# Kernel optimization log

Measured on AMD Instinct MI355X. Metric: run time of the kernel, lower is better.

Reference implementation:

```python
import jax, jax.numpy as jnp
import numpy as np

N_CUMULANTS = 3  # forward() calls compute_cumulants_fwd(values, 3)
P = 576
N_ROWS = 200000
PROJ_DIMS = 4


def setup_inputs() -> dict:
    key = jax.random.key(0)
    k1, k2, k3 = jax.random.split(key, 3)
    X = jax.random.normal(k1, (N_ROWS, P), dtype=jnp.float32)
    mu = jax.random.normal(k2, (P * N_CUMULANTS,), dtype=jnp.float32)
    W = jax.random.normal(k3, (P * N_CUMULANTS, PROJ_DIMS), dtype=jnp.float32)
    return {"X": X, "mu": mu, "W": W}


def _cumulants(X):
    # X: (N, P). Vectorized version of the per-column torch loop.
    # n_cumulants = 3: c0 = mean, c1 = mean(centered^1), c2 = mean(centered^2)
    m = jnp.mean(X, axis=0)                 # (P,)
    centered = X - m                        # (N, P)
    mom1 = jnp.mean(centered, axis=0)       # (P,) ~0 numerically, kept for faithfulness
    mom2 = jnp.mean(centered * centered, axis=0)  # (P,) variance
    # layout matches out[:, jbase:jbase+n_cumulants]: interleave per feature column
    c = jnp.stack([m, mom1, mom2], axis=1)  # (P, 3)
    return c.reshape(1, -1)                 # (1, P*3)


def reference(X, mu, W):
    cum = _cumulants(X.astype(jnp.float32))          # (1, P*3)
    projected = jnp.einsum('ij,jk->ik', cum - mu, W)  # (1, PROJ_DIMS)
    return projected
```

## Files before the change

kernel.cpp:

```cpp
#include <hip/hip_runtime.h>

#define N_ROWS 200000
#define P 576
#define P4 144
#define GRID1 1024


__global__ __launch_bounds__(576) void colsum_kernel(const float4* __restrict__ X4,
                                                     float* __restrict__ S1,
                                                     float* __restrict__ S2) {
    const int x = threadIdx.x;
    const int y = threadIdx.y;

    float4 s1 = make_float4(0.f, 0.f, 0.f, 0.f);
    float4 s2 = make_float4(0.f, 0.f, 0.f, 0.f);

    for (int r = blockIdx.x * 4 + y; r < N_ROWS; r += GRID1 * 4) {
        float4 v = X4[(size_t)r * P4 + x];
        s1.x += v.x;      s1.y += v.y;      s1.z += v.z;      s1.w += v.w;
        s2.x += v.x * v.x; s2.y += v.y * v.y; s2.z += v.z * v.z; s2.w += v.w * v.w;
    }

    __shared__ float4 sh1[4][P4];
    __shared__ float4 sh2[4][P4];
    sh1[y][x] = s1;
    sh2[y][x] = s2;
    __syncthreads();

    if (y == 0) {
        #pragma unroll
        for (int i = 1; i < 4; ++i) {
            float4 a = sh1[i][x], b = sh2[i][x];
            s1.x += a.x; s1.y += a.y; s1.z += a.z; s1.w += a.w;
            s2.x += b.x; s2.y += b.y; s2.z += b.z; s2.w += b.w;
        }
        atomicAdd(&S1[4 * x + 0], s1.x);
        atomicAdd(&S1[4 * x + 1], s1.y);
        atomicAdd(&S1[4 * x + 2], s1.z);
        atomicAdd(&S1[4 * x + 3], s1.w);
        atomicAdd(&S2[4 * x + 0], s2.x);
        atomicAdd(&S2[4 * x + 1], s2.y);
        atomicAdd(&S2[4 * x + 2], s2.z);
        atomicAdd(&S2[4 * x + 3], s2.w);
    }
}

__global__ __launch_bounds__(256) void project_kernel(const float* __restrict__ S1,
                                                      const float* __restrict__ S2,
                                                      const float* __restrict__ mu,
                                                      const float* __restrict__ W,
                                                      float* __restrict__ out) {
    const int tid = threadIdx.x;
    const float invN = 1.0f / (float)N_ROWS;
    float acc0 = 0.f, acc1 = 0.f, acc2 = 0.f, acc3 = 0.f;

    for (int p = tid; p < P; p += 256) {
        float m    = S1[p] * invN;
        float mom2 = S2[p] * invN - m * m;
        int j = 3 * p;
        float c0 = m    - mu[j];
        float c1 = 0.f  - mu[j + 1];
        float c2 = mom2 - mu[j + 2];
        const float* w0 = &W[(size_t)j * 4];
        acc0 += c0 * w0[0] + c1 * w0[4] + c2 * w0[8];
        acc1 += c0 * w0[1] + c1 * w0[5] + c2 * w0[9];
        acc2 += c0 * w0[2] + c1 * w0[6] + c2 * w0[10];
        acc3 += c0 * w0[3] + c1 * w0[7] + c2 * w0[11];
    }

    #pragma unroll
    for (int off = 32; off > 0; off >>= 1) {
        acc0 += __shfl_down(acc0, off);
        acc1 += __shfl_down(acc1, off);
        acc2 += __shfl_down(acc2, off);
        acc3 += __shfl_down(acc3, off);
    }

    __shared__ float sacc[4][4];
    const int wave = tid >> 6;
    const int lane = tid & 63;
    if (lane == 0) {
        sacc[wave][0] = acc0;
        sacc[wave][1] = acc1;
        sacc[wave][2] = acc2;
        sacc[wave][3] = acc3;
    }
    __syncthreads();
    if (tid < 4) {
        float r = sacc[0][tid] + sacc[1][tid] + sacc[2][tid] + sacc[3][tid];
        out[tid] = r;
    }
}

extern "C" void kernel_launch(void* const* d_in, const int* in_sizes, int n_in,
                              void* d_out, int out_size, void* d_ws, size_t ws_size,
                              hipStream_t stream) {
    const float* X  = (const float*)d_in[0];
    const float* mu = (const float*)d_in[1];
    const float* W  = (const float*)d_in[2];
    float* out = (float*)d_out;

    float* S1 = (float*)d_ws;
    float* S2 = S1 + P;

    hipMemsetAsync(d_ws, 0, 2 * P * sizeof(float), stream);

    dim3 block(P4, 4);
    colsum_kernel<<<GRID1, block, 0, stream>>>((const float4*)X, S1, S2);
    project_kernel<<<1, 256, 0, stream>>>(S1, S2, mu, W, out);
}
```

Baseline: 654.4 us.

## Fuse projection into column-sum kernel via last-block ticket; use nontemporal loads

Merges the two kernels into one. After its atomics, each block takes a ticket from a global counter, and the last block to finish reads the final column sums and computes the projection, which removes a second kernel launch. Streaming reads of X now use nontemporal loads through ext_vector_type float4. The price is a threadfence plus a serialized tail in one block, and correctness now depends on the counter being zeroed by the memset.

```diff
diff --git a/kernel.cpp b/kernel.cpp
--- a/kernel.cpp
+++ b/kernel.cpp
@@ -5,24 +5,31 @@
 #define P4 144
 #define GRID1 1024
 
+typedef float floatx4 __attribute__((ext_vector_type(4)));
 
-__global__ __launch_bounds__(576) void colsum_kernel(const float4* __restrict__ X4,
-                                                     float* __restrict__ S1,
-                                                     float* __restrict__ S2) {
+
+__global__ __launch_bounds__(576) void fused_kernel(const floatx4* __restrict__ X4,
+                                                    const float* __restrict__ mu,
+                                                    const float* __restrict__ W,
+                                                    float* __restrict__ S1,
+                                                    float* __restrict__ S2,
+                                                    unsigned int* __restrict__ counter,
+                                                    float* __restrict__ out) {
     const int x = threadIdx.x;
     const int y = threadIdx.y;
+    const int tid = y * P4 + x;
 
-    float4 s1 = make_float4(0.f, 0.f, 0.f, 0.f);
-    float4 s2 = make_float4(0.f, 0.f, 0.f, 0.f);
+    floatx4 s1 = {0.f, 0.f, 0.f, 0.f};
+    floatx4 s2 = {0.f, 0.f, 0.f, 0.f};
 
     for (int r = blockIdx.x * 4 + y; r < N_ROWS; r += GRID1 * 4) {
-        float4 v = X4[(size_t)r * P4 + x];
-        s1.x += v.x;      s1.y += v.y;      s1.z += v.z;      s1.w += v.w;
-        s2.x += v.x * v.x; s2.y += v.y * v.y; s2.z += v.z * v.z; s2.w += v.w * v.w;
+        floatx4 v = __builtin_nontemporal_load(&X4[(size_t)r * P4 + x]);
+        s1 += v;
+        s2 += v * v;
     }
 
-    __shared__ float4 sh1[4][P4];
-    __shared__ float4 sh2[4][P4];
+    __shared__ floatx4 sh1[4][P4];
+    __shared__ floatx4 sh2[4][P4];
     sh1[y][x] = s1;
     sh2[y][x] = s2;
     __syncthreads();
@@ -30,9 +37,8 @@
     if (y == 0) {
         #pragma unroll
         for (int i = 1; i < 4; ++i) {
-            float4 a = sh1[i][x], b = sh2[i][x];
-            s1.x += a.x; s1.y += a.y; s1.z += a.z; s1.w += a.w;
-            s2.x += b.x; s2.y += b.y; s2.z += b.z; s2.w += b.w;
+            s1 += sh1[i][x];
+            s2 += sh2[i][x];
         }
         atomicAdd(&S1[4 * x + 0], s1.x);
         atomicAdd(&S1[4 * x + 1], s1.y);
@@ -43,43 +49,48 @@
         atomicAdd(&S2[4 * x + 2], s2.z);
         atomicAdd(&S2[4 * x + 3], s2.w);
     }
-}
 
-__global__ __launch_bounds__(256) void project_kernel(const float* __restrict__ S1,
-                                                      const float* __restrict__ S2,
-                                                      const float* __restrict__ mu,
-                                                      const float* __restrict__ W,
-                                                      float* __restrict__ out) {
-    const int tid = threadIdx.x;
+    __threadfence();
+    __shared__ unsigned int ticket;
+    __syncthreads();
+    if (tid == 0) ticket = atomicAdd(counter, 1u);
+    __syncthreads();
+    if (ticket != GRID1 - 1) return;
+
+    __threadfence();
+
     const float invN = 1.0f / (float)N_ROWS;
     float acc0 = 0.f, acc1 = 0.f, acc2 = 0.f, acc3 = 0.f;
 
-    for (int p = tid; p < P; p += 256) {
-        float m    = S1[p] * invN;
-        float mom2 = S2[p] * invN - m * m;
-        int j = 3 * p;
-        float c0 = m    - mu[j];
-        float c1 = 0.f  - mu[j + 1];
-        float c2 = mom2 - mu[j + 2];
-        const float* w0 = &W[(size_t)j * 4];
-        acc0 += c0 * w0[0] + c1 * w0[4] + c2 * w0[8];
-        acc1 += c0 * w0[1] + c1 * w0[5] + c2 * w0[9];
-        acc2 += c0 * w0[2] + c1 * w0[6] + c2 * w0[10];
-        acc3 += c0 * w0[3] + c1 * w0[7] + c2 * w0[11];
-    }
-
-    #pragma unroll
-    for (int off = 32; off > 0; off >>= 1) {
-        acc0 += __shfl_down(acc0, off);
-        acc1 += __shfl_down(acc1, off);
-        acc2 += __shfl_down(acc2, off);
-        acc3 += __shfl_down(acc3, off);
+    if (tid < 256) {
+        for (int p = tid; p < P; p += 256) {
+            float sv1 = atomicAdd(&S1[p], 0.0f);
+            float sv2 = atomicAdd(&S2[p], 0.0f);
+            float m    = sv1 * invN;
+            float mom2 = sv2 * invN - m * m;
+            int j = 3 * p;
+            float c0 = m    - mu[j];
+            float c1 = 0.f  - mu[j + 1];
+            float c2 = mom2 - mu[j + 2];
+            const float* w0 = &W[(size_t)j * 4];
+            acc0 += c0 * w0[0] + c1 * w0[4] + c2 * w0[8];
+            acc1 += c0 * w0[1] + c1 * w0[5] + c2 * w0[9];
+            acc2 += c0 * w0[2] + c1 * w0[6] + c2 * w0[10];
+            acc3 += c0 * w0[3] + c1 * w0[7] + c2 * w0[11];
+        }
+        #pragma unroll
+        for (int off = 32; off > 0; off >>= 1) {
+            acc0 += __shfl_down(acc0, off);
+            acc1 += __shfl_down(acc1, off);
+            acc2 += __shfl_down(acc2, off);
+            acc3 += __shfl_down(acc3, off);
+        }
     }
 
     __shared__ float sacc[4][4];
     const int wave = tid >> 6;
     const int lane = tid & 63;
-    if (lane == 0) {
+    if (tid < 256 && lane == 0) {
         sacc[wave][0] = acc0;
         sacc[wave][1] = acc1;
         sacc[wave][2] = acc2;
@@ -87,8 +98,7 @@
     }
     __syncthreads();
     if (tid < 4) {
-        float r = sacc[0][tid] + sacc[1][tid] + sacc[2][tid] + sacc[3][tid];
-        out[tid] = r;
+        out[tid] = sacc[0][tid] + sacc[1][tid] + sacc[2][tid] + sacc[3][tid];
     }
 }
 
@@ -102,10 +112,11 @@
 
     float* S1 = (float*)d_ws;
     float* S2 = S1 + P;
+    unsigned int* counter = (unsigned int*)(S2 + P);
 
-    hipMemsetAsync(d_ws, 0, 2 * P * sizeof(float), stream);
+    (void)hipMemsetAsync(d_ws, 0, (2 * P + 1) * sizeof(float), stream);
 
     dim3 block(P4, 4);
-    colsum_kernel<<<GRID1, block, 0, stream>>>((const float4*)X, S1, S2);
-    project_kernel<<<1, 256, 0, stream>>>(S1, S2, mu, W, out);
+    fused_kernel<<<GRID1, block, 0, stream>>>((const floatx4*)X, mu, W,
+                                              S1, S2, counter, out);
 }
```

Result: slower. 809.6 us (+23.7%).
